# Performance work log

Hardware: AMD Instinct MI355X
Metric: run time of the kernel (lower is better)

The kernel has to match this reference:

```python
import jax, jax.numpy as jnp
import numpy as np

INPUT, HIDDEN, OUTPUT = 512, 1024, 512
BATCH, SEQ = 128, 256


def setup_inputs() -> dict:
    key = jax.random.key(0)
    ks = jax.random.split(key, 14)
    s_in = 1.0 / np.sqrt(INPUT)
    s_h = 1.0 / np.sqrt(HIDDEN)
    d = {
        "x_seq": jax.random.normal(ks[0], (BATCH, SEQ, INPUT), jnp.float32),
        "Wxf_w": jax.random.uniform(ks[1], (HIDDEN, INPUT), jnp.float32, -s_in, s_in),
        "Wxf_b": jax.random.uniform(ks[2], (HIDDEN,), jnp.float32, -s_in, s_in),
        "Whf_w": jax.random.uniform(ks[3], (HIDDEN, HIDDEN), jnp.float32, -s_h, s_h),
        "Wxi_w": jax.random.uniform(ks[4], (HIDDEN, INPUT), jnp.float32, -s_in, s_in),
        "Wxi_b": jax.random.uniform(ks[5], (HIDDEN,), jnp.float32, -s_in, s_in),
        "Whi_w": jax.random.uniform(ks[6], (HIDDEN, HIDDEN), jnp.float32, -s_h, s_h),
        "Wxg_w": jax.random.uniform(ks[7], (HIDDEN, INPUT), jnp.float32, -s_in, s_in),
        "Wxg_b": jax.random.uniform(ks[8], (HIDDEN,), jnp.float32, -s_in, s_in),
        "Whg_w": jax.random.uniform(ks[9], (HIDDEN, HIDDEN), jnp.float32, -s_h, s_h),
        "Wxo_w": jax.random.uniform(ks[10], (HIDDEN, INPUT), jnp.float32, -s_in, s_in),
        "Wxo_b": jax.random.uniform(ks[11], (HIDDEN,), jnp.float32, -s_in, s_in),
        "Who_w": jax.random.uniform(ks[12], (HIDDEN, HIDDEN), jnp.float32, -s_h, s_h),
        "Why_w": jax.random.uniform(ks[13], (OUTPUT, HIDDEN), jnp.float32, -s_h, s_h),
        "Why_b": jnp.zeros((OUTPUT,), jnp.float32),
    }
    return d


def _lstm(x_seq, Wxf_w, Wxf_b, Whf_w, Wxi_w, Wxi_b, Whi_w,
          Wxg_w, Wxg_b, Whg_w, Wxo_w, Wxo_b, Who_w, Why_w, Why_b):
    batch, seq_len, _ = x_seq.shape
    hidden = Whf_w.shape[0]
    # Precompute input projections for all timesteps (one big GEMM per gate).
    xf = jnp.einsum('bsi,hi->bsh', x_seq, Wxf_w) + Wxf_b  # (B,S,H)
    xi = jnp.einsum('bsi,hi->bsh', x_seq, Wxi_w) + Wxi_b
    xg = jnp.einsum('bsi,hi->bsh', x_seq, Wxg_w) + Wxg_b
    xo = jnp.einsum('bsi,hi->bsh', x_seq, Wxo_w) + Wxo_b
    # time-major for scan: (S, B, H)
    xs = jnp.stack([xf, xi, xg, xo], axis=0).transpose(2, 0, 1, 3)  # (S,4,B,H)

    h0 = jnp.zeros((batch, hidden), x_seq.dtype)
    c0 = jnp.zeros((batch, hidden), x_seq.dtype)

    def step(carry, x_t):
        h, c = carry
        xf_t, xi_t, xg_t, xo_t = x_t[0], x_t[1], x_t[2], x_t[3]
        f_t = jax.nn.sigmoid(xf_t + h @ Whf_w.T)
        i_t = jax.nn.sigmoid(xi_t + h @ Whi_w.T)
        g_t = jnp.tanh(xg_t + h @ Whg_w.T)
        c = f_t * c + i_t * g_t
        o_t = jax.nn.sigmoid(xo_t + h @ Who_w.T)
        h = o_t * jnp.tanh(c)
        return (h, c), None

    (h, c), _ = jax.lax.scan(step, (h0, c0), xs)
    out = h @ Why_w.T + Why_b
    return out, h, c


def reference(x_seq, Wxf_w, Wxf_b, Whf_w, Wxi_w, Wxi_b, Whi_w,
              Wxg_w, Wxg_b, Whg_w, Wxo_w, Wxo_b, Who_w, Why_w, Why_b):
    return _lstm(x_seq, Wxf_w, Wxf_b, Whf_w, Wxi_w, Wxi_b, Whi_w,
                 Wxg_w, Wxg_b, Whg_w, Wxo_w, Wxo_b, Who_w, Why_w, Why_b)
```

## Files before the change

kernel.cpp:

```cpp
#include <hip/hip_runtime.h>


#define B_ 128
#define S_ 256
#define I_ 512
#define H_ 1024
#define O_ 512

typedef unsigned short u16;
typedef unsigned int u32;
typedef unsigned long long u64;

typedef short v8s __attribute__((ext_vector_type(8)));
typedef float v16f __attribute__((ext_vector_type(16)));
typedef float v4f __attribute__((ext_vector_type(4)));

__device__ __forceinline__ u16 f2bf(float f) {
  u32 u = __float_as_uint(f);
  u32 r = (u + 0x7fffu + ((u >> 16) & 1u)) >> 16;
  return (u16)r;
}
__device__ __forceinline__ u32 pack2(float a, float b) {
  return (u32)f2bf(a) | ((u32)f2bf(b) << 16);
}
__device__ __forceinline__ uint4 cvt8(const float* __restrict__ s) {
  float4 f0 = ((const float4*)s)[0];
  float4 f1 = ((const float4*)s)[1];
  uint4 o;
  o.x = pack2(f0.x, f0.y); o.y = pack2(f0.z, f0.w);
  o.z = pack2(f1.x, f1.y); o.w = pack2(f1.z, f1.w);
  return o;
}

__device__ __forceinline__ uint4 uc_ld16(const u16* p) {
  u64 lo = __hip_atomic_load((const u64*)p, __ATOMIC_RELAXED, __HIP_MEMORY_SCOPE_AGENT);
  u64 hi = __hip_atomic_load((const u64*)p + 1, __ATOMIC_RELAXED, __HIP_MEMORY_SCOPE_AGENT);
  uint4 v; v.x = (u32)lo; v.y = (u32)(lo >> 32); v.z = (u32)hi; v.w = (u32)(hi >> 32);
  return v;
}
__device__ __forceinline__ void uc_st16(u16* p, uint4 v) {
  u64 lo = (u64)v.x | ((u64)v.y << 32);
  u64 hi = (u64)v.z | ((u64)v.w << 32);
  __hip_atomic_store((u64*)p, lo, __ATOMIC_RELAXED, __HIP_MEMORY_SCOPE_AGENT);
  __hip_atomic_store((u64*)p + 1, hi, __ATOMIC_RELAXED, __HIP_MEMORY_SCOPE_AGENT);
}

__global__ void lstm_prep(
    const float* __restrict__ x,
    const float* __restrict__ Whf, const float* __restrict__ Whi,
    const float* __restrict__ Whg, const float* __restrict__ Who,
    const float* __restrict__ Wxf, const float* __restrict__ Wxi,
    const float* __restrict__ Wxg, const float* __restrict__ Wxo,
    const float* __restrict__ bfp, const float* __restrict__ bip,
    const float* __restrict__ bgp, const float* __restrict__ bop,
    const float* __restrict__ Why,
    u16* __restrict__ xt, u16* __restrict__ Wc, float* __restrict__ bc,
    u16* __restrict__ WhyT, u16* __restrict__ hbuf, u32* __restrict__ barrier)
{
  const int gid = blockIdx.x * blockDim.x + threadIdx.x;
  const int gsz = gridDim.x * blockDim.x;

  if (gid < 256) barrier[gid] = 0u;

  for (int v = gid; v < (S_ * B_ * I_ / 8); v += gsz) {
    int flat = v * 8;
    int b = flat / (S_ * I_);
    int rem = flat - b * (S_ * I_);
    int t = rem / I_;
    int i = rem - t * I_;
    size_t dst = ((size_t)(t * 4 + (b >> 5)) * 64 + (i >> 3)) * 32 + (b & 31);
    ((uint4*)xt)[dst] = cvt8(x + flat);
  }

  for (int o = gid; o < 192 * 4096; o += gsz) {
    int w8 = o >> 12;
    int colG = o & 4095;
    int unit = ((colG >> 6) << 4) + (((colG >> 5) & 1) << 3) + ((colG >> 2) & 7);
    int g = colG & 3;
    const float* Whp = (g == 0) ? Whf : (g == 1) ? Whi : (g == 2) ? Whg : Who;
    const float* Wxp = (g == 0) ? Wxf : (g == 1) ? Wxi : (g == 2) ? Wxg : Wxo;
    const float* s = (w8 < 64) ? (Wxp + (size_t)unit * 512 + w8 * 8)
                               : (Whp + (size_t)unit * 1024 + (w8 - 64) * 8);
    ((uint4*)Wc)[o] = cvt8(s);
  }

  for (int n = gid; n < 4096; n += gsz) {
    int unit = ((n >> 6) << 4) + (((n >> 5) & 1) << 3) + ((n >> 2) & 7);
    int g = n & 3;
    const float* bp = (g == 0) ? bfp : (g == 1) ? bip : (g == 2) ? bgp : bop;
    bc[n] = bp[unit];
  }

  for (int v = gid; v < (O_ * H_ / 8); v += gsz) {
    int flat = v * 8;
    *(uint4*)(WhyT + flat) = cvt8(Why + flat);
  }

  for (int v = gid; v < 2 * 16384; v += gsz) {
    uint4 z; z.x = 0; z.y = 0; z.z = 0; z.w = 0;
    ((uint4*)hbuf)[v] = z;
  }
}

__global__ __launch_bounds__(256, 1) void lstm_seq(
    const u16* __restrict__ xt, const u16* __restrict__ Wc,
    const float* __restrict__ bc, u16* __restrict__ hbuf,
    const u16* __restrict__ WhyT, const float* __restrict__ WhyB,
    float* __restrict__ out, u32* __restrict__ barrier, int rotFlag)
{
  __shared__ float scr[2048];
  __shared__ u16 hstage[512];

  const int tid  = threadIdx.x;
  const int lane = tid & 63;
  const int w    = tid >> 6;
  const int ct   = w & 1;
  const int kh   = w >> 1;
  const int rq   = blockIdx.x >> 6;
  const int cg   = blockIdx.x & 63;
  const bool rot = (rotFlag != 0);

  const int colN  = lane & 31;
  const int kgsel = lane >> 5;
  const int colG  = cg * 64 + ct * 32 + colN;
  const int gate  = colN & 3;
  const int unitL = ct * 8 + (colN >> 2);
  const float bias = bc[colG];

  const uint4* xA4  = (const uint4*)xt;
  const uint4* WcF4 = (const uint4*)Wc;
  uint4*       HA4  = (uint4*)hbuf;

  const int xaOff = rq * 2048 + kh * 1024 + lane;
  const int xbOff = kh * 131072 + kgsel * 4096 + colG;
  const int haOff = rq * 4096 + kh * 2048 + lane;
  const int hbOff = 262144 + kh * 262144 + kgsel * 4096 + colG;

  float c[8];
#pragma unroll
  for (int i = 0; i < 8; ++i) c[i] = 0.f;

  __builtin_amdgcn_fence(__ATOMIC_ACQUIRE, "agent");
  __syncthreads();

  v8s Bx[16], Bh[32];
  {
    const uint4* bx = WcF4 + xbOff;
#pragma unroll
    for (int kb = 0; kb < 16; ++kb)
      Bx[kb] = __builtin_bit_cast(v8s, bx[(size_t)kb * 8192]);
    const uint4* bh = WcF4 + hbOff;
#pragma unroll
    for (int kb = 0; kb < 32; ++kb)
      Bh[kb] = __builtin_bit_cast(v8s, bh[(size_t)kb * 8192]);
  }

  v16f acc0, acc1;

#pragma unroll 1
  for (int t = 0; t < S_; ++t) {
    const size_t tb = rot ? (size_t)t * 16384 : (size_t)(t & 1) * 16384;
    const size_t tn = rot ? (size_t)(t + 1) * 16384 : (size_t)((t & 1) ^ 1) * 16384;

#pragma unroll
    for (int i = 0; i < 16; ++i) { acc0[i] = 0.f; acc1[i] = 0.f; }

    {
      const uint4* ax = xA4 + (size_t)t * 8192 + xaOff;
      v8s xr[16];
#pragma unroll
      for (int kb = 0; kb < 16; ++kb)
        xr[kb] = __builtin_bit_cast(v8s, ax[kb * 64]);
#pragma unroll
      for (int kb = 0; kb < 16; ++kb) {
        if (kb & 1) acc1 = __builtin_amdgcn_mfma_f32_32x32x16_bf16(xr[kb], Bx[kb], acc1, 0, 0, 0);
        else        acc0 = __builtin_amdgcn_mfma_f32_32x32x16_bf16(xr[kb], Bx[kb], acc0, 0, 0, 0);
      }
    }

    if (t > 0) {
      if (tid < 64) {
        u32 spins = 0;
        while (__hip_atomic_load(&barrier[rq * 64 + tid], __ATOMIC_RELAXED,
                                 __HIP_MEMORY_SCOPE_AGENT) < (u32)t) {
          __builtin_amdgcn_s_sleep(1);
          if (++spins > (1u << 22)) break;
        }
      }
      __syncthreads();
    }

    {
      const uint4* ah = HA4 + tb + haOff;
      v8s hr[32];
      if (rot) {
#pragma unroll
        for (int kb = 0; kb < 32; ++kb)
          hr[kb] = __builtin_bit_cast(v8s, ah[kb * 64]);
      } else {
#pragma unroll
        for (int kb = 0; kb < 32; ++kb)
          hr[kb] = __builtin_bit_cast(v8s, uc_ld16((const u16*)(ah + kb * 64)));
      }
#pragma unroll
      for (int kb = 0; kb < 32; ++kb) {
        if (kb & 1) acc1 = __builtin_amdgcn_mfma_f32_32x32x16_bf16(hr[kb], Bh[kb], acc1, 0, 0, 0);
        else        acc0 = __builtin_amdgcn_mfma_f32_32x32x16_bf16(hr[kb], Bh[kb], acc0, 0, 0, 0);
      }
    }

    float aT[16];
#pragma unroll
    for (int i = 0; i < 16; ++i) aT[i] = acc0[i] + acc1[i];
    {
      int h2 = 1 - kh;
#pragma unroll
      for (int i = 0; i < 8; ++i)
        scr[ct * 1024 + h2 * 512 + i * 64 + lane] = aT[h2 * 8 + i];
    }
    __syncthreads();

    const bool lastT = (t == S_ - 1);
#pragma unroll
    for (int i = 0; i < 8; ++i) {
      int r = kh * 8 + i;
      float pre = aT[r] + scr[ct * 1024 + kh * 512 + i * 64 + lane] + bias;
      float e = __expf((gate == 2) ? (2.f * pre) : (-pre));
      float act = (gate == 2) ? (1.f - 2.f / (e + 1.f)) : (1.f / (1.f + e));
      int qb = lane & ~3;
      float F = __shfl(act, qb + 0, 64);
      float I = __shfl(act, qb + 1, 64);
      float G = __shfl(act, qb + 2, 64);
      float O = __shfl(act, qb + 3, 64);
      float cn = fmaf(F, c[i], I * G);
      c[i] = cn;
      float e2 = __expf(2.f * cn);
      float hv = O * (1.f - 2.f / (e2 + 1.f));
      if (gate == 0) {
        int rowL = (r & 3) + ((r >> 2) << 3) + (kgsel << 2);
        hstage[rowL * 16 + unitL] = f2bf(hv);
        if (lastT) {
          int grow = rq * 32 + rowL;
          int gunit = cg * 16 + unitL;
          out[65536 + grow * H_ + gunit] = hv;
          out[196608 + grow * H_ + gunit] = cn;
        }
      }
    }
    __syncthreads();

    if (tid < 64) {
      int row = tid >> 1, u16sel = tid & 1;
      uint4 v = ((const uint4*)hstage)[tid];
      uc_st16((u16*)(HA4 + tn + rq * 4096 + (size_t)(2 * cg + u16sel) * 32 + row), v);
      asm volatile("s_waitcnt vmcnt(0)" ::: "memory");
      if (tid == 0)
        __hip_atomic_store(&barrier[rq * 64 + cg], (u32)(t + 1), __ATOMIC_RELAXED,
                           __HIP_MEMORY_SCOPE_AGENT);
    }
  }

  {
    u32 spins = 0;
    while (__hip_atomic_load(&barrier[tid], __ATOMIC_RELAXED,
                             __HIP_MEMORY_SCOPE_AGENT) < (u32)S_) {
      __builtin_amdgcn_s_sleep(2);
      if (++spins > (1u << 22)) break;
    }
  }
  __syncthreads();

  if (blockIdx.x < 32) {
    const int wg = blockIdx.x;
    const uint4* HF = HA4 + (rot ? (size_t)S_ * 16384 : 0);
    const int l15 = lane & 15;
    const int l4 = lane >> 4;
    const int colO = (wg << 4) + l15;
    v4f o0, o1;
#pragma unroll
    for (int i = 0; i < 4; ++i) { o0[i] = 0.f; o1[i] = 0.f; }
#pragma unroll 4
    for (int kc = 0; kc < 32; ++kc) {
      v8s bfrag = *(const v8s*)(WhyT + (size_t)colO * H_ + kc * 32 + (l4 << 3));
      size_t i0 = (size_t)w * 4096 + kc * 128 + l4 * 32 + l15;
      v8s a0, a1;
      if (rot) {
        a0 = __builtin_bit_cast(v8s, HF[i0]);
        a1 = __builtin_bit_cast(v8s, HF[i0 + 16]);
      } else {
        a0 = __builtin_bit_cast(v8s, uc_ld16((const u16*)(HF + i0)));
        a1 = __builtin_bit_cast(v8s, uc_ld16((const u16*)(HF + i0 + 16)));
      }
      o0 = __builtin_amdgcn_mfma_f32_16x16x32_bf16(a0, bfrag, o0, 0, 0, 0);
      o1 = __builtin_amdgcn_mfma_f32_16x16x32_bf16(a1, bfrag, o1, 0, 0, 0);
    }
    float bO = WhyB[colO];
#pragma unroll
    for (int r2 = 0; r2 < 4; ++r2) {
      int row = (w << 5) + (l4 << 2) + r2;
      out[row * O_ + colO] = o0[r2] + bO;
      out[(row + 16) * O_ + colO] = o1[r2] + bO;
    }
  }
}

extern "C" void kernel_launch(void* const* d_in, const int* in_sizes, int n_in,
                              void* d_out, int out_size, void* d_ws, size_t ws_size,
                              hipStream_t stream) {
  const float* x    = (const float*)d_in[0];
  const float* Wxf  = (const float*)d_in[1];
  const float* bf_  = (const float*)d_in[2];
  const float* Whf  = (const float*)d_in[3];
  const float* Wxi  = (const float*)d_in[4];
  const float* bi_  = (const float*)d_in[5];
  const float* Whi  = (const float*)d_in[6];
  const float* Wxg  = (const float*)d_in[7];
  const float* bg_  = (const float*)d_in[8];
  const float* Whg  = (const float*)d_in[9];
  const float* Wxo  = (const float*)d_in[10];
  const float* bo_  = (const float*)d_in[11];
  const float* Who  = (const float*)d_in[12];
  const float* Why  = (const float*)d_in[13];
  const float* Whyb = (const float*)d_in[14];

  char* ws = (char*)d_ws;
  u16*   xtp  = (u16*)(ws);
  u16*   Wcp  = (u16*)(ws + 33554432);
  float* bcp  = (float*)(ws + 46137344);
  u16*   WhyT = (u16*)(ws + 46153728);
  u32*   barp = (u32*)(ws + 47202304);
  u16*   hbuf = (u16*)(ws + 47203328);
  float* outp = (float*)d_out;

  const size_t need_rot = 47203328ull + 257ull * 262144ull;
  int rot = (ws_size >= need_rot) ? 1 : 0;

  lstm_prep<<<dim3(1024), dim3(256), 0, stream>>>(
      x, Whf, Whi, Whg, Who, Wxf, Wxi, Wxg, Wxo,
      bf_, bi_, bg_, bo_, Why, xtp, Wcp, bcp, WhyT, hbuf, barp);

  lstm_seq<<<dim3(256), dim3(256), 0, stream>>>(
      xtp, Wcp, bcp, hbuf, WhyT, Whyb, outp, barp, rot);
}
```

Measured before the change: 2.098 ms.

## Switch to per-wave barrier flags and drop block-level syncs in LSTM step

Replaces the per-block barrier counter with per-wave flags (4 per block), so each wave publishes its own h slice directly to global memory and signals readiness without the trailing __syncthreads and single-wave store. Waiting waves poll only the flags for the k-half they consume, using 64-bit loads that check two flags at once, and no longer block-sync after the wait. The scratch buffer is double-buffered by timestep parity to make removing those syncs safe. This aims to cut the serial latency of the per-step cross-block handoff, at the cost of more flag traffic and a larger barrier region.

New measurement: 2.477 ms. +18.1%, slower.

```diff
diff --git a/kernel.cpp b/kernel.cpp
--- a/kernel.cpp
+++ b/kernel.cpp
@@ -60,7 +60,7 @@
   const int gid = blockIdx.x * blockDim.x + threadIdx.x;
   const int gsz = gridDim.x * blockDim.x;
 
-  if (gid < 256) barrier[gid] = 0u;
+  if (gid < 1024) barrier[gid] = 0u;
 
   for (int v = gid; v < (S_ * B_ * I_ / 8); v += gsz) {
     int flat = v * 8;
@@ -108,8 +108,8 @@
     const u16* __restrict__ WhyT, const float* __restrict__ WhyB,
     float* __restrict__ out, u32* __restrict__ barrier, int rotFlag)
 {
-  __shared__ float scr[2048];
-  __shared__ u16 hstage[512];
+  __shared__ float scr[4096];
+  __shared__ u16 hws[512];
 
   const int tid  = threadIdx.x;
   const int lane = tid & 63;
@@ -179,15 +179,15 @@
     }
 
     if (t > 0) {
-      if (tid < 64) {
-        u32 spins = 0;
-        while (__hip_atomic_load(&barrier[rq * 64 + tid], __ATOMIC_RELAXED,
-                                 __HIP_MEMORY_SCOPE_AGENT) < (u32)t) {
-          __builtin_amdgcn_s_sleep(1);
-          if (++spins > (1u << 22)) break;
-        }
-      }
-      __syncthreads();
+      const u64* fb = (const u64*)(barrier + rq * 256 + kh * 128);
+      u32 spins = 0;
+      for (;;) {
+        u64 v = __hip_atomic_load(fb + lane, __ATOMIC_RELAXED,
+                                  __HIP_MEMORY_SCOPE_AGENT);
+        if ((u32)v >= (u32)t && (u32)(v >> 32) >= (u32)t) break;
+        __builtin_amdgcn_s_sleep(1);
+        if (++spins > (1u << 22)) break;
+      }
     }
 
     {
@@ -212,11 +212,12 @@
     float aT[16];
 #pragma unroll
     for (int i = 0; i < 16; ++i) aT[i] = acc0[i] + acc1[i];
+    float* scrT = scr + ((t & 1) << 11);
     {
       int h2 = 1 - kh;
 #pragma unroll
       for (int i = 0; i < 8; ++i)
-        scr[ct * 1024 + h2 * 512 + i * 64 + lane] = aT[h2 * 8 + i];
+        scrT[ct * 1024 + h2 * 512 + i * 64 + lane] = aT[h2 * 8 + i];
     }
     __syncthreads();
 
@@ -224,7 +225,7 @@
 #pragma unroll
     for (int i = 0; i < 8; ++i) {
       int r = kh * 8 + i;
-      float pre = aT[r] + scr[ct * 1024 + kh * 512 + i * 64 + lane] + bias;
+      float pre = aT[r] + scrT[ct * 1024 + kh * 512 + i * 64 + lane] + bias;
       float e = __expf((gate == 2) ? (2.f * pre) : (-pre));
       float act = (gate == 2) ? (1.f - 2.f / (e + 1.f)) : (1.f / (1.f + e));
       int qb = lane & ~3;
@@ -238,7 +239,7 @@
       float hv = O * (1.f - 2.f / (e2 + 1.f));
       if (gate == 0) {
         int rowL = (r & 3) + ((r >> 2) << 3) + (kgsel << 2);
-        hstage[rowL * 16 + unitL] = f2bf(hv);
+        hws[(w << 7) + ((rowL & 15) << 3) + (colN >> 2)] = f2bf(hv);
         if (lastT) {
           int grow = rq * 32 + rowL;
           int gunit = cg * 16 + unitL;
@@ -246,26 +247,31 @@
           out[196608 + grow * H_ + gunit] = cn;
         }
       }
-    }
-    __syncthreads();
-
-    if (tid < 64) {
-      int row = tid >> 1, u16sel = tid & 1;
-      uint4 v = ((const uint4*)hstage)[tid];
-      uc_st16((u16*)(HA4 + tn + rq * 4096 + (size_t)(2 * cg + u16sel) * 32 + row), v);
-      asm volatile("s_waitcnt vmcnt(0)" ::: "memory");
-      if (tid == 0)
-        __hip_atomic_store(&barrier[rq * 64 + cg], (u32)(t + 1), __ATOMIC_RELAXED,
-                           __HIP_MEMORY_SCOPE_AGENT);
-    }
+      if (lane < 2) {
+        int R = (r & 3) + ((r >> 2) << 3) + (lane << 2);
+        uint4 vv = *(const uint4*)(hws + (w << 7) + ((R & 15) << 3));
+        uc_st16((u16*)(HA4 + tn + rq * 4096 + (size_t)(2 * cg + ct) * 32 + R), vv);
+      }
+    }
+
+    asm volatile("s_waitcnt vmcnt(0)" ::: "memory");
+    if (lane == 0)
+      __hip_atomic_store(&barrier[rq * 256 + cg * 4 + w], (u32)(t + 1),
+                         __ATOMIC_RELAXED, __HIP_MEMORY_SCOPE_AGENT);
   }
 
   {
-    u32 spins = 0;
-    while (__hip_atomic_load(&barrier[tid], __ATOMIC_RELAXED,
-                             __HIP_MEMORY_SCOPE_AGENT) < (u32)S_) {
-      __builtin_amdgcn_s_sleep(2);
-      if (++spins > (1u << 22)) break;
+    const u64* fb = (const u64*)barrier;
+#pragma unroll 1
+    for (int k = tid; k < 512; k += 256) {
+      u32 spins = 0;
+      for (;;) {
+        u64 v = __hip_atomic_load(fb + k, __ATOMIC_RELAXED,
+                                  __HIP_MEMORY_SCOPE_AGENT);
+        if ((u32)v >= (u32)S_ && (u32)(v >> 32) >= (u32)S_) break;
+        __builtin_amdgcn_s_sleep(2);
+        if (++spins > (1u << 22)) break;
+      }
     }
   }
   __syncthreads();
@@ -329,10 +335,10 @@
   float* bcp  = (float*)(ws + 46137344);
   u16*   WhyT = (u16*)(ws + 46153728);
   u32*   barp = (u32*)(ws + 47202304);
-  u16*   hbuf = (u16*)(ws + 47203328);
+  u16*   hbuf = (u16*)(ws + 47206400);
   float* outp = (float*)d_out;
 
-  const size_t need_rot = 47203328ull + 257ull * 262144ull;
+  const size_t need_rot = 47206400ull + 257ull * 262144ull;
   int rot = (ws_size >= need_rot) ? 1 : 0;
 
   lstm_prep<<<dim3(1024), dim3(256), 0, stream>>>(
```
